# Kernel tuning notes

Hardware: AMD Instinct MI355X
Metric: run time of the kernel (lower is better)

## Reference

```python
import jax, jax.numpy as jnp
import numpy as np

L_OUTPUT = 1024  # SequenceDecoder l_output


def setup_inputs() -> dict:
    key = jax.random.key(0)
    k1, k2, k3 = jax.random.split(key, 3)
    B, L, D, DO = 16, 4096, 1024, 1024
    x = jax.random.normal(k1, (B, L, D), dtype=jnp.float32)
    # 0/1 padding-style mask; valid_length = mask.sum(axis=1)
    attention_mask = jax.random.randint(k2, (B, L), 0, 2, dtype=jnp.int32)
    # nn.Linear(d_model, d_output): weight (DO, D), bias (DO,)
    W = jax.random.normal(k3, (DO, D), dtype=jnp.float32) * (1.0 / np.sqrt(D))
    b = jnp.zeros((DO,), dtype=jnp.float32)
    return {"x": x, "attention_mask": attention_mask, "W": W, "b": b}


def _restrict_last(x, attention_mask, l_output):
    """Vectorized equivalent of the per-sample Python loop in mode='last':
    for each batch row i, take the LAST s_i = min(valid_len_i, l_output)
    elements of the full sequence, zero-padded at the tail to l_output.
    (When all s_i == l_output this matches x[:, -l_output:, :], which is the
    only case the original torch.stack-based loop handles without error.)"""
    B, L, D = x.shape
    valid = attention_mask.sum(axis=1)                    # (B,)
    s = jnp.minimum(valid, l_output)                      # (B,)
    j = jnp.arange(l_output)                              # (l_output,)
    idx = jnp.clip(L - s[:, None] + j[None, :], 0, L - 1) # (B, l_output)
    gathered = jnp.take_along_axis(x, idx[:, :, None], axis=1)  # (B, l_output, D)
    keep = (j[None, :] < s[:, None])[:, :, None]          # (B, l_output, 1)
    return jnp.where(keep, gathered, jnp.zeros((), dtype=x.dtype))


def reference(x, attention_mask, W, b):
    # mode='last' restrict, then output_transform = nn.Linear(d_model, d_output)
    restricted = _restrict_last(x, attention_mask, L_OUTPUT)  # (B, l_output, D)
    return jnp.einsum('bld,od->blo', restricted, W) + b       # (B, l_output, DO)
```

## Files before the change

### kernel.cpp

```cpp
#include <hip/hip_runtime.h>
#include <hip/hip_bf16.h>

#define L_SEQ   4096
#define D_IN    1024
#define N_BATCH 16
#define L_OUT   1024
#define D_OUT   1024
#define M_DIM   (N_BATCH * L_OUT)
#define K_DIM   D_IN

#define BM 256
#define BN 256
#define BK 64
#define NKT (K_DIM / BK)

typedef __attribute__((ext_vector_type(4))) float  f32x4;
typedef __attribute__((ext_vector_type(8))) __bf16 bf16x8;
typedef __attribute__((ext_vector_type(4))) __bf16 bf16x4;

#define WS_A_OFF 0u
#define WS_W_OFF (32u * 1024u * 1024u)
#define WS_S_OFF (WS_W_OFF + 2u * 1024u * 1024u)

__global__ __launch_bounds__(256) void mask_sum_kernel(
    const int* __restrict__ mask, int* __restrict__ s_out)
{
    const int b = blockIdx.x;
    const int t = threadIdx.x;
    const int* row = mask + (size_t)b * L_SEQ;

    int sum = 0;
#pragma unroll
    for (int i = 0; i < L_SEQ / 256; ++i) sum += row[t + i * 256];

#pragma unroll
    for (int off = 32; off > 0; off >>= 1) sum += __shfl_down(sum, off, 64);

    __shared__ int wsum[4];
    if ((t & 63) == 0) wsum[t >> 6] = sum;
    __syncthreads();
    if (t == 0) {
        int total = wsum[0] + wsum[1] + wsum[2] + wsum[3];
        s_out[b] = total < L_OUT ? total : L_OUT;
    }
}

__global__ __launch_bounds__(256) void convert_kernel(
    const float* __restrict__ x,
    const float* __restrict__ W,
    const int*   __restrict__ s_arr,
    __bf16* __restrict__ wsA,
    __bf16* __restrict__ wsW)
{
    const int rid = blockIdx.x;
    const int t   = threadIdx.x;
    const int e0  = t * 4;

    if (rid < M_DIM) {
        const int b = rid >> 10;
        const int j = rid & (L_OUT - 1);
        const int s = s_arr[b];
        const int rsw  = (rid & 7) << 3;
        const int dste = (e0 & ~63) | ((e0 & 63) ^ rsw);
        __bf16* dst = wsA + (size_t)rid * K_DIM + dste;
        if (j < s) {
            const float* src = x + ((size_t)b * L_SEQ + (L_SEQ - s + j)) * D_IN + e0;
            f32x4 v = *(const f32x4*)src;
            bf16x4 o = {(__bf16)v.x, (__bf16)v.y, (__bf16)v.z, (__bf16)v.w};
            *(bf16x4*)dst = o;
        } else {
            bf16x4 o = {(__bf16)0.f, (__bf16)0.f, (__bf16)0.f, (__bf16)0.f};
            *(bf16x4*)dst = o;
        }
    } else {
        const int n = rid - M_DIM;
        const int rsw  = (n & 7) << 3;
        const int dste = (e0 & ~63) | ((e0 & 63) ^ rsw);
        const float* src = W + (size_t)n * D_IN + e0;
        f32x4 v = *(const f32x4*)src;
        bf16x4 o = {(__bf16)v.x, (__bf16)v.y, (__bf16)v.z, (__bf16)v.w};
        *(bf16x4*)(wsW + (size_t)n * K_DIM + dste) = o;
    }
}

__device__ __forceinline__ void gload16(const __bf16* g, __bf16* l) {
    __builtin_amdgcn_global_load_lds(
        (const __attribute__((address_space(1))) void*)g,
        (__attribute__((address_space(3))) void*)l,
        16, 0, 0);
}

#define FENCE() asm volatile("" ::: "memory")

__global__ __launch_bounds__(512, 2) void gemm_kernel(
    const __bf16* __restrict__ A,
    const __bf16* __restrict__ Wb,
    const float*  __restrict__ bias,
    float* __restrict__ out)
{
    __shared__ __bf16 smem[2][2][BM * BK];

    const int t  = threadIdx.x;
    const int bx = blockIdx.x;
    const int tile_n = bx & 3;
    const int tile_m = bx >> 2;
    const int m0 = tile_m * BM;
    const int n0 = tile_n * BN;
    const int lane = t & 63;
    const int wave = t >> 6;
    const int wm = wave >> 2;
    const int wn = wave & 3;

    const int srow = t >> 3;
    const int scol = (t & 7) * 8;
    const int sdst = (t & 7) * 8;

    const __bf16* Ag = A  + (size_t)m0 * K_DIM;
    const __bf16* Bg = Wb + (size_t)n0 * K_DIM;

#define STAGE_HALF(gbase, lbase, h, kt_)                                   \
    {                                                                      \
        _Pragma("unroll")                                                  \
        for (int rd = 0; rd < 2; ++rd) {                                   \
            const int r_ = (h) * 128 + rd * 64 + srow;                     \
            gload16((gbase) + (size_t)r_ * K_DIM + (kt_) * BK + scol,      \
                    (lbase) + r_ * BK + sdst);                             \
        }                                                                  \
    }

    const int fr  = lane & 15;
    const int k8  = (lane >> 4) * 8;
    const int swz = (fr & 7) << 3;
    const int kc0 = k8 ^ swz;
    const int kc1 = (32 + k8) ^ swz;

    bf16x8 aF[4][2], bF0[2][2], bF1[2][2];
    f32x4 acc[8][4];
#pragma unroll
    for (int f = 0; f < 8; ++f)
#pragma unroll
        for (int g = 0; g < 4; ++g) acc[f][g] = (f32x4){0.f, 0.f, 0.f, 0.f};

#define LOAD_AF(Ac, mh)                                                    \
    {                                                                      \
        const __bf16* rb_ = (Ac) + (wm * 128 + (mh) * 64 + fr) * BK;       \
        _Pragma("unroll")                                                  \
        for (int i = 0; i < 4; ++i) {                                      \
            aF[i][0] = *(const bf16x8*)&rb_[i * 16 * BK + kc0];            \
            aF[i][1] = *(const bf16x8*)&rb_[i * 16 * BK + kc1];            \
        }                                                                  \
    }

#define LOAD_BF(Bc, nh, bF)                                                \
    {                                                                      \
        const __bf16* rb_ = (Bc) + (wn * 64 + (nh) * 32 + fr) * BK;        \
        _Pragma("unroll")                                                  \
        for (int j = 0; j < 2; ++j) {                                      \
            bF[j][0] = *(const bf16x8*)&rb_[j * 16 * BK + kc0];            \
            bF[j][1] = *(const bf16x8*)&rb_[j * 16 * BK + kc1];            \
        }                                                                  \
    }

#define MFMA_QUAD(mh, nh, bF)                                              \
    {                                                                      \
        _Pragma("unroll")                                                  \
        for (int i = 0; i < 4; ++i)                                        \
            _Pragma("unroll")                                              \
            for (int j = 0; j < 2; ++j) {                                  \
                f32x4 c_ = acc[(mh) * 4 + i][(nh) * 2 + j];                \
                c_ = __builtin_amdgcn_mfma_f32_16x16x32_bf16(              \
                    aF[i][0], bF[j][0], c_, 0, 0, 0);                      \
                c_ = __builtin_amdgcn_mfma_f32_16x16x32_bf16(              \
                    aF[i][1], bF[j][1], c_, 0, 0, 0);                      \
                acc[(mh) * 4 + i][(nh) * 2 + j] = c_;                      \
            }                                                              \
    }

    {
        __bf16* A0l = &smem[0][0][0];
        __bf16* B0l = &smem[0][1][0];
        __bf16* A1l = &smem[1][0][0];
        __bf16* B1l = &smem[1][1][0];
        STAGE_HALF(Ag, A0l, 0, 0);
        STAGE_HALF(Bg, B0l, 1, 0);
        STAGE_HALF(Ag, A0l, 1, 0);
        STAGE_HALF(Bg, B0l, 0, 0);
        STAGE_HALF(Ag, A1l, 0, 1);
        STAGE_HALF(Bg, B1l, 1, 1);
    }

    for (int kt = 0; kt < NKT; ++kt) {
        const int cur = kt & 1;
        __bf16* Ac = &smem[cur][0][0];
        __bf16* Bc = &smem[cur][1][0];
        __bf16* An = &smem[cur ^ 1][0][0];
        __bf16* Bn = &smem[cur ^ 1][1][0];

        FENCE();
        if (kt == NKT - 1) asm volatile("s_waitcnt vmcnt(0)" ::: "memory");
        else               asm volatile("s_waitcnt vmcnt(4)" ::: "memory");
        __builtin_amdgcn_s_barrier();
        FENCE();
        LOAD_AF(Ac, 0);
        LOAD_BF(Bc, 0, bF0);
        if (kt + 1 < NKT) {
            STAGE_HALF(Ag, An, 1, kt + 1);
            STAGE_HALF(Bg, Bn, 0, kt + 1);
        }
        asm volatile("s_waitcnt lgkmcnt(0)" ::: "memory");
        __builtin_amdgcn_sched_barrier(0);
        __builtin_amdgcn_s_setprio(1);
        MFMA_QUAD(0, 0, bF0);
        __builtin_amdgcn_s_setprio(0);

        FENCE();
        __builtin_amdgcn_s_barrier();
        FENCE();
        LOAD_BF(Bc, 1, bF1);
        asm volatile("s_waitcnt lgkmcnt(0)" ::: "memory");
        __builtin_amdgcn_sched_barrier(0);
        __builtin_amdgcn_s_setprio(1);
        MFMA_QUAD(0, 1, bF1);
        __builtin_amdgcn_s_setprio(0);

        FENCE();
        __builtin_amdgcn_s_barrier();
        FENCE();
        LOAD_AF(Ac, 1);
        if (kt + 2 < NKT) STAGE_HALF(Ag, Ac, 0, kt + 2);
        asm volatile("s_waitcnt lgkmcnt(0)" ::: "memory");
        __builtin_amdgcn_sched_barrier(0);
        __builtin_amdgcn_s_setprio(1);
        MFMA_QUAD(1, 1, bF1);
        __builtin_amdgcn_s_setprio(0);

        FENCE();
        __builtin_amdgcn_s_barrier();
        FENCE();
        if (kt + 2 < NKT) STAGE_HALF(Bg, Bc, 1, kt + 2);
        __builtin_amdgcn_s_setprio(1);
        MFMA_QUAD(1, 0, bF0);
        __builtin_amdgcn_s_setprio(0);
    }

    float bias_v[4];
#pragma unroll
    for (int g = 0; g < 4; ++g)
        bias_v[g] = bias[n0 + wn * 64 + g * 16 + fr];

    const int row0 = m0 + wm * 128 + (lane >> 4) * 4;
    const int col0 = n0 + wn * 64 + fr;
#pragma unroll
    for (int f = 0; f < 8; ++f)
#pragma unroll
        for (int g = 0; g < 4; ++g)
#pragma unroll
            for (int rr = 0; rr < 4; ++rr)
                out[(size_t)(row0 + f * 16 + rr) * D_OUT + (col0 + g * 16)] =
                    acc[f][g][rr] + bias_v[g];

#undef STAGE_HALF
#undef LOAD_AF
#undef LOAD_BF
#undef MFMA_QUAD
}

extern "C" void kernel_launch(void* const* d_in, const int* in_sizes, int n_in,
                              void* d_out, int out_size, void* d_ws, size_t ws_size,
                              hipStream_t stream) {
    const float* x    = (const float*)d_in[0];
    const int*   mask = (const int*)d_in[1];
    const float* W    = (const float*)d_in[2];
    const float* bias = (const float*)d_in[3];
    float*       out  = (float*)d_out;

    __bf16* wsA   = (__bf16*)((char*)d_ws + WS_A_OFF);
    __bf16* wsW   = (__bf16*)((char*)d_ws + WS_W_OFF);
    int*    s_arr = (int*)((char*)d_ws + WS_S_OFF);

    mask_sum_kernel<<<dim3(N_BATCH), dim3(256), 0, stream>>>(mask, s_arr);

    convert_kernel<<<dim3(M_DIM + D_OUT), dim3(256), 0, stream>>>(
        x, W, s_arr, wsA, wsW);

    const int grid = (M_DIM / BM) * (D_OUT / BN);
    gemm_kernel<<<dim3(grid), dim3(512), 0, stream>>>(wsA, wsW, bias, out);
}
```

Before: 63.98 us.

## Fuse gather and bf16 conversion of x into GEMM A-tile staging

The separate conversion pass that gathered the last rows of x into a bf16 workspace is removed. The GEMM now loads fp32 x rows directly into registers, masks them, converts them to bf16 and writes them swizzled into LDS, interleaved with the MFMA phases. The mask-sum and W conversion are merged into one small prep kernel. This saves a 64MB read and 32MB write round trip plus a launch. The cost is more registers and VALU work inside the GEMM, fp32 global loads that are twice as wide, and A prefetch going through registers instead of direct-to-LDS loads.

```diff
diff --git a/kernel.cpp b/kernel.cpp
--- a/kernel.cpp
+++ b/kernel.cpp
@@ -18,62 +18,34 @@
 typedef __attribute__((ext_vector_type(8))) __bf16 bf16x8;
 typedef __attribute__((ext_vector_type(4))) __bf16 bf16x4;
 
-#define WS_A_OFF 0u
-#define WS_W_OFF (32u * 1024u * 1024u)
-#define WS_S_OFF (WS_W_OFF + 2u * 1024u * 1024u)
-
-__global__ __launch_bounds__(256) void mask_sum_kernel(
-    const int* __restrict__ mask, int* __restrict__ s_out)
-{
-    const int b = blockIdx.x;
-    const int t = threadIdx.x;
-    const int* row = mask + (size_t)b * L_SEQ;
-
-    int sum = 0;
-#pragma unroll
-    for (int i = 0; i < L_SEQ / 256; ++i) sum += row[t + i * 256];
-
-#pragma unroll
-    for (int off = 32; off > 0; off >>= 1) sum += __shfl_down(sum, off, 64);
-
-    __shared__ int wsum[4];
-    if ((t & 63) == 0) wsum[t >> 6] = sum;
-    __syncthreads();
-    if (t == 0) {
-        int total = wsum[0] + wsum[1] + wsum[2] + wsum[3];
-        s_out[b] = total < L_OUT ? total : L_OUT;
-    }
-}
-
-__global__ __launch_bounds__(256) void convert_kernel(
-    const float* __restrict__ x,
+#define WS_W_OFF 0u
+#define WS_S_OFF (4u * 1024u * 1024u)
+
+__global__ __launch_bounds__(256) void prep_kernel(
+    const int*   __restrict__ mask,
     const float* __restrict__ W,
-    const int*   __restrict__ s_arr,
-    __bf16* __restrict__ wsA,
+    int*    __restrict__ s_out,
     __bf16* __restrict__ wsW)
 {
-    const int rid = blockIdx.x;
-    const int t   = threadIdx.x;
-    const int e0  = t * 4;
-
-    if (rid < M_DIM) {
-        const int b = rid >> 10;
-        const int j = rid & (L_OUT - 1);
-        const int s = s_arr[b];
-        const int rsw  = (rid & 7) << 3;
-        const int dste = (e0 & ~63) | ((e0 & 63) ^ rsw);
-        __bf16* dst = wsA + (size_t)rid * K_DIM + dste;
-        if (j < s) {
-            const float* src = x + ((size_t)b * L_SEQ + (L_SEQ - s + j)) * D_IN + e0;
-            f32x4 v = *(const f32x4*)src;
-            bf16x4 o = {(__bf16)v.x, (__bf16)v.y, (__bf16)v.z, (__bf16)v.w};
-            *(bf16x4*)dst = o;
-        } else {
-            bf16x4 o = {(__bf16)0.f, (__bf16)0.f, (__bf16)0.f, (__bf16)0.f};
-            *(bf16x4*)dst = o;
+    const int t = threadIdx.x;
+    if (blockIdx.x < 16) {
+        const int b = blockIdx.x;
+        const int* row = mask + (size_t)b * L_SEQ;
+        int sum = 0;
+#pragma unroll
+        for (int i = 0; i < L_SEQ / 256; ++i) sum += row[t + i * 256];
+#pragma unroll
+        for (int off = 32; off > 0; off >>= 1) sum += __shfl_down(sum, off, 64);
+        __shared__ int wsum[4];
+        if ((t & 63) == 0) wsum[t >> 6] = sum;
+        __syncthreads();
+        if (t == 0) {
+            int total = wsum[0] + wsum[1] + wsum[2] + wsum[3];
+            s_out[b] = total < L_OUT ? total : L_OUT;
         }
     } else {
-        const int n = rid - M_DIM;
+        const int n  = blockIdx.x - 16;
+        const int e0 = t * 4;
         const int rsw  = (n & 7) << 3;
         const int dste = (e0 & ~63) | ((e0 & 63) ^ rsw);
         const float* src = W + (size_t)n * D_IN + e0;
@@ -93,12 +65,14 @@
 #define FENCE() asm volatile("" ::: "memory")
 
 __global__ __launch_bounds__(512, 2) void gemm_kernel(
-    const __bf16* __restrict__ A,
+    const float*  __restrict__ x,
     const __bf16* __restrict__ Wb,
     const float*  __restrict__ bias,
+    const int*    __restrict__ s_arr,
     float* __restrict__ out)
 {
-    __shared__ __bf16 smem[2][2][BM * BK];
+    __shared__ __bf16 sA[2][BM * BK];
+    __shared__ __bf16 sB[2][BN * BK];
 
     const int t  = threadIdx.x;
     const int bx = blockIdx.x;
@@ -113,18 +87,52 @@
 
     const int srow = t >> 3;
     const int scol = (t & 7) * 8;
-    const int sdst = (t & 7) * 8;
-
-    const __bf16* Ag = A  + (size_t)m0 * K_DIM;
     const __bf16* Bg = Wb + (size_t)n0 * K_DIM;
 
-#define STAGE_HALF(gbase, lbase, h, kt_)                                   \
+#define STAGE_B_HALF(dstB, h, kt_)                                         \
     {                                                                      \
         _Pragma("unroll")                                                  \
         for (int rd = 0; rd < 2; ++rd) {                                   \
             const int r_ = (h) * 128 + rd * 64 + srow;                     \
-            gload16((gbase) + (size_t)r_ * K_DIM + (kt_) * BK + scol,      \
-                    (lbase) + r_ * BK + sdst);                             \
+            gload16(Bg + (size_t)r_ * K_DIM + (kt_) * BK + scol,           \
+                    (dstB) + r_ * BK + scol);                              \
+        }                                                                  \
+    }
+
+    const int ar = t >> 4;
+    const int ac = (t & 15) * 4;
+    const int bb = tile_m >> 2;
+    const int s  = s_arr[bb];
+    const int jbase = (tile_m & 3) * 256;
+    const float* xb = x + (size_t)bb * L_SEQ * D_IN + (size_t)(L_SEQ - s) * D_IN;
+
+    int aoff[8];
+#pragma unroll
+    for (int l = 0; l < 8; ++l) {
+        const int j  = jbase + ar + 32 * l;
+        const int jc = (j < s) ? j : 0;
+        aoff[l] = jc * D_IN + ac;
+    }
+
+    f32x4 areg[8];
+    const f32x4 zf = {0.f, 0.f, 0.f, 0.f};
+
+#define ISSUE_A(kt_)                                                       \
+    {                                                                      \
+        _Pragma("unroll")                                                  \
+        for (int l = 0; l < 8; ++l)                                        \
+            areg[l] = *(const f32x4*)(xb + aoff[l] + (kt_) * BK);          \
+    }
+
+#define CVT_A(dstA, l0_)                                                   \
+    {                                                                      \
+        _Pragma("unroll")                                                  \
+        for (int l = (l0_); l < (l0_) + 4; ++l) {                          \
+            const int j_   = jbase + ar + 32 * l;                          \
+            const int row_ = ar + 32 * l;                                  \
+            f32x4 v = (j_ < s) ? areg[l] : zf;                             \
+            bf16x4 o = {(__bf16)v.x, (__bf16)v.y, (__bf16)v.z, (__bf16)v.w}; \
+            *(bf16x4*)&(dstA)[row_ * BK + (ac ^ ((row_ & 7) << 3))] = o;   \
         }                                                                  \
     }
 
@@ -176,71 +184,70 @@
             }                                                              \
     }
 
-    {
-        __bf16* A0l = &smem[0][0][0];
-        __bf16* B0l = &smem[0][1][0];
-        __bf16* A1l = &smem[1][0][0];
-        __bf16* B1l = &smem[1][1][0];
-        STAGE_HALF(Ag, A0l, 0, 0);
-        STAGE_HALF(Bg, B0l, 1, 0);
-        STAGE_HALF(Ag, A0l, 1, 0);
-        STAGE_HALF(Bg, B0l, 0, 0);
-        STAGE_HALF(Ag, A1l, 0, 1);
-        STAGE_HALF(Bg, B1l, 1, 1);
-    }
+    ISSUE_A(0);
+    STAGE_B_HALF(sB[0], 0, 0);
+    STAGE_B_HALF(sB[0], 1, 0);
+    CVT_A(sA[0], 0);
+    CVT_A(sA[0], 4);
+    ISSUE_A(1);
+    asm volatile("s_waitcnt lgkmcnt(0)" ::: "memory");
+    __builtin_amdgcn_sched_barrier(0);
 
     for (int kt = 0; kt < NKT; ++kt) {
         const int cur = kt & 1;
-        __bf16* Ac = &smem[cur][0][0];
-        __bf16* Bc = &smem[cur][1][0];
-        __bf16* An = &smem[cur ^ 1][0][0];
-        __bf16* Bn = &smem[cur ^ 1][1][0];
+        __bf16* Ac = sA[cur];
+        __bf16* Bc = sB[cur];
+        __bf16* An = sA[cur ^ 1];
+        __bf16* Bn = sB[cur ^ 1];
 
         FENCE();
         if (kt == NKT - 1) asm volatile("s_waitcnt vmcnt(0)" ::: "memory");
-        else               asm volatile("s_waitcnt vmcnt(4)" ::: "memory");
+        else               asm volatile("s_waitcnt vmcnt(8)" ::: "memory");
         __builtin_amdgcn_s_barrier();
         FENCE();
         LOAD_AF(Ac, 0);
         LOAD_BF(Bc, 0, bF0);
+        asm volatile("s_waitcnt lgkmcnt(0)" ::: "memory");
+        __builtin_amdgcn_sched_barrier(0);
+        __builtin_amdgcn_s_setprio(1);
+        MFMA_QUAD(0, 0, bF0);
+        __builtin_amdgcn_s_setprio(0);
+
+        FENCE();
+        __builtin_amdgcn_s_barrier();
+        FENCE();
+        if (kt + 1 < NKT) STAGE_B_HALF(Bn, 0, kt + 1);
+        LOAD_BF(Bc, 1, bF1);
+        asm volatile("s_waitcnt lgkmcnt(0)" ::: "memory");
+        __builtin_amdgcn_sched_barrier(0);
+        __builtin_amdgcn_s_setprio(1);
+        MFMA_QUAD(0, 1, bF1);
+        __builtin_amdgcn_s_setprio(0);
+
+        FENCE();
+        __builtin_amdgcn_s_barrier();
+        FENCE();
+        LOAD_AF(Ac, 1);
+        if (kt + 1 < NKT) CVT_A(An, 0);
+        asm volatile("s_waitcnt lgkmcnt(0)" ::: "memory");
+        __builtin_amdgcn_sched_barrier(0);
+        __builtin_amdgcn_s_setprio(1);
+        MFMA_QUAD(1, 1, bF1);
+        __builtin_amdgcn_s_setprio(0);
+
+        FENCE();
+        __builtin_amdgcn_s_barrier();
+        FENCE();
         if (kt + 1 < NKT) {
-            STAGE_HALF(Ag, An, 1, kt + 1);
-            STAGE_HALF(Bg, Bn, 0, kt + 1);
+            STAGE_B_HALF(Bn, 1, kt + 1);
+            CVT_A(An, 4);
         }
-        asm volatile("s_waitcnt lgkmcnt(0)" ::: "memory");
-        __builtin_amdgcn_sched_barrier(0);
-        __builtin_amdgcn_s_setprio(1);
-        MFMA_QUAD(0, 0, bF0);
-        __builtin_amdgcn_s_setprio(0);
-
-        FENCE();
-        __builtin_amdgcn_s_barrier();
-        FENCE();
-        LOAD_BF(Bc, 1, bF1);
-        asm volatile("s_waitcnt lgkmcnt(0)" ::: "memory");
-        __builtin_amdgcn_sched_barrier(0);
-        __builtin_amdgcn_s_setprio(1);
-        MFMA_QUAD(0, 1, bF1);
-        __builtin_amdgcn_s_setprio(0);
-
-        FENCE();
-        __builtin_amdgcn_s_barrier();
-        FENCE();
-        LOAD_AF(Ac, 1);
-        if (kt + 2 < NKT) STAGE_HALF(Ag, Ac, 0, kt + 2);
-        asm volatile("s_waitcnt lgkmcnt(0)" ::: "memory");
-        __builtin_amdgcn_sched_barrier(0);
-        __builtin_amdgcn_s_setprio(1);
-        MFMA_QUAD(1, 1, bF1);
-        __builtin_amdgcn_s_setprio(0);
-
-        FENCE();
-        __builtin_amdgcn_s_barrier();
-        FENCE();
-        if (kt + 2 < NKT) STAGE_HALF(Bg, Bc, 1, kt + 2);
+        if (kt + 2 < NKT) ISSUE_A(kt + 2);
         __builtin_amdgcn_s_setprio(1);
         MFMA_QUAD(1, 0, bF0);
         __builtin_amdgcn_s_setprio(0);
+        asm volatile("s_waitcnt lgkmcnt(0)" ::: "memory");
+        __builtin_amdgcn_sched_barrier(0);
     }
 
     float bias_v[4];
@@ -259,7 +266,9 @@
                 out[(size_t)(row0 + f * 16 + rr) * D_OUT + (col0 + g * 16)] =
                     acc[f][g][rr] + bias_v[g];
 
-#undef STAGE_HALF
+#undef STAGE_B_HALF
+#undef ISSUE_A
+#undef CVT_A
 #undef LOAD_AF
 #undef LOAD_BF
 #undef MFMA_QUAD
@@ -274,15 +283,13 @@
     const float* bias = (const float*)d_in[3];
     float*       out  = (float*)d_out;
 
-    __bf16* wsA   = (__bf16*)((char*)d_ws + WS_A_OFF);
     __bf16* wsW   = (__bf16*)((char*)d_ws + WS_W_OFF);
     int*    s_arr = (int*)((char*)d_ws + WS_S_OFF);
 
-    mask_sum_kernel<<<dim3(N_BATCH), dim3(256), 0, stream>>>(mask, s_arr);
-
-    convert_kernel<<<dim3(M_DIM + D_OUT), dim3(256), 0, stream>>>(
-        x, W, s_arr, wsA, wsW);
+    prep_kernel<<<dim3(16 + D_OUT), dim3(256), 0, stream>>>(
+        mask, W, s_arr, wsW);
 
     const int grid = (M_DIM / BM) * (D_OUT / BN);
-    gemm_kernel<<<dim3(grid), dim3(512), 0, stream>>>(wsA, wsW, bias, out);
-}
+    gemm_kernel<<<dim3(grid), dim3(512), 0, stream>>>(
+        x, wsW, bias, s_arr, out);
+}
```

New measurement: 78.75 us. 23.1% more time.
